# Optimization experiments

Hardware: AMD Instinct MI355X
Metric: run time of the kernel (lower is better)

Reference implementation:

```python
import jax, jax.numpy as jnp
import numpy as np
import math

EMBED_DIM = 2048
NUM_HEADS = 16
D_K = 128
BSZ = 2
SEQ = 2048


def make_freq_pos_enc(dim, max_seq_len):
    # inv_freq over dim/2 freqs, then interleave-repeat each freq twice: (f r), r=2
    inv_freq = 1.0 / (10000.0 ** (jnp.arange(0, dim, 2, dtype=jnp.float32) / dim))
    pos = jnp.arange(max_seq_len, dtype=jnp.float32)
    pe = jnp.einsum('p,f->pf', pos, inv_freq)                 # [S, dim/2]
    return jnp.repeat(pe, 2, axis=-1)                          # [S, dim], pattern (f r)


def rotate_half(u):
    # pairs are interleaved: (..., d r) with r=2
    u = u.reshape(*u.shape[:-1], -1, 2)
    u1, u2 = u[..., 0], u[..., 1]
    return jnp.stack((-u2, u1), axis=-1).reshape(*u.shape[:-2], -1)


def rotate(u, pos_enc):
    pe = pos_enc[: u.shape[-2]]                                # [S, d_k]
    return u * jnp.cos(pe) + rotate_half(u) * jnp.sin(pe)


def setup_inputs() -> dict:
    key = jax.random.key(0)
    ks = jax.random.split(key, 5)
    scale = 1.0 / math.sqrt(EMBED_DIM)
    return {
        'x': jax.random.normal(ks[0], (BSZ, SEQ, EMBED_DIM), dtype=jnp.float32),
        'wq': jax.random.normal(ks[1], (NUM_HEADS * D_K, EMBED_DIM), dtype=jnp.float32) * scale,
        'wk': jax.random.normal(ks[2], (NUM_HEADS * D_K, EMBED_DIM), dtype=jnp.float32) * scale,
        'wv': jax.random.normal(ks[3], (NUM_HEADS * D_K, EMBED_DIM), dtype=jnp.float32) * scale,
        'wo': jax.random.normal(ks[4], (EMBED_DIM, NUM_HEADS * D_K), dtype=jnp.float32) * scale,
        'freq_pos_enc': make_freq_pos_enc(D_K, SEQ),
        'mask': jnp.zeros((SEQ, SEQ), dtype=jnp.float32),  # dead arg in original forward
        'num_heads': NUM_HEADS,
        'd_k': D_K,
    }


def reference(x, wq, wk, wv, wo, freq_pos_enc, mask, num_heads, d_k):
    bsz, seq_len, _ = x.shape
    # projections (nn.Linear, no bias): x @ W^T
    def proj(w):
        p = jnp.einsum('bse,de->bsd', x, w)
        return p.reshape(bsz, seq_len, num_heads, d_k).transpose(0, 2, 1, 3)  # [B,H,S,d]
    q, k, v = proj(wq), proj(wk), proj(wv)
    q, k = rotate(q, freq_pos_enc), rotate(k, freq_pos_enc)
    # regenerated causal mask (0 on/below diagonal, -inf above)
    causal = jnp.where(
        jnp.arange(seq_len)[:, None] >= jnp.arange(seq_len)[None, :],
        0.0, -jnp.inf).astype(x.dtype)
    scores = jnp.einsum('bhsd,bhtd->bhst', q, k) / math.sqrt(d_k) + causal
    weights = jax.nn.softmax(scores, axis=-1)
    attn = jnp.einsum('bhst,bhtd->bhsd', weights, v)           # [B,H,S,d]
    attn = attn.transpose(0, 2, 1, 3).reshape(bsz, seq_len, -1)
    return jnp.einsum('bsd,ed->bse', attn, wo)


if __name__ == '__main__':
    out = reference(**setup_inputs())
    print(out.shape, out.dtype)
```

## Files before the change

kernel.cpp:

```cpp
#include <hip/hip_runtime.h>


typedef unsigned short u16;
typedef unsigned int   u32;
typedef __attribute__((ext_vector_type(4)))  float f32x4;
typedef __attribute__((ext_vector_type(16))) float f32x16;
typedef __attribute__((ext_vector_type(8)))  short short8;
typedef __attribute__((ext_vector_type(4)))  u16   u16x4;
typedef __attribute__((ext_vector_type(2)))  u16   u16x2;

#define NB   2
#define NH   16
#define SEQ  2048
#define DK   128
#define EMB  2048

__device__ __forceinline__ u16 f2bf(float f) {
    union { float f; unsigned int u; } v; v.f = f;
    unsigned int r = v.u + 0x7FFFu + ((v.u >> 16) & 1u);
    return (u16)(r >> 16);
}
__device__ __forceinline__ float bf2f(u16 h) {
    union { unsigned int u; float f; } v; v.u = ((unsigned int)h) << 16;
    return v.f;
}
__device__ __forceinline__ f32x4 mfma16(short8 a, short8 b, f32x4 c) {
    return __builtin_amdgcn_mfma_f32_16x16x32_bf16(a, b, c, 0, 0, 0);
}
__device__ __forceinline__ f32x16 mfma32(short8 a, short8 b, f32x16 c) {
    return __builtin_amdgcn_mfma_f32_32x32x16_bf16(a, b, c, 0, 0, 0);
}

#define GLDS(gsrc, ldst) __builtin_amdgcn_global_load_lds( \
    (const __attribute__((address_space(1))) void*)(gsrc), \
    (__attribute__((address_space(3))) void*)(ldst), 16, 0, 0)

__global__ __launch_bounds__(256) void cast_f32_bf16(const float* __restrict__ in,
                                                     u16* __restrict__ out, int n4) {
    int i = blockIdx.x * 256 + threadIdx.x;
    if (i >= n4) return;
    f32x4 v = ((const f32x4*)in)[i];
    u16x4 o;
    o[0] = f2bf(v[0]); o[1] = f2bf(v[1]); o[2] = f2bf(v[2]); o[3] = f2bf(v[3]);
    ((u16x4*)out)[i] = o;
}

__global__ __launch_bounds__(256) void rope_table(const float* __restrict__ freq,
                                                  float* __restrict__ ct,
                                                  float* __restrict__ st) {
    int i = blockIdx.x * 256 + threadIdx.x;
    int s = i >> 6, d2 = i & 63;
    float pe = freq[s * DK + d2 * 2];
    ct[i] = cosf(pe);
    st[i] = sinf(pe);
}

__global__ __launch_bounds__(256) void rope_apply(u16* __restrict__ Qb, u16* __restrict__ Kb,
                                                  const float* __restrict__ ct,
                                                  const float* __restrict__ st) {
    int i = blockIdx.x * 256 + threadIdx.x;
    int d2 = i & 63;
    int s  = (i >> 6) & (SEQ - 1);
    float c  = ct[(s << 6) + d2];
    float sn = st[(s << 6) + d2];
    size_t off = (size_t)i * 2;
    u16x2 q = *(const u16x2*)(Qb + off);
    float q0 = bf2f(q[0]), q1 = bf2f(q[1]);
    u16x2 qo; qo[0] = f2bf(q0 * c - q1 * sn); qo[1] = f2bf(q1 * c + q0 * sn);
    *(u16x2*)(Qb + off) = qo;
    u16x2 k = *(const u16x2*)(Kb + off);
    float k0 = bf2f(k[0]), k1 = bf2f(k[1]);
    u16x2 ko; ko[0] = f2bf(k0 * c - k1 * sn); ko[1] = f2bf(k1 * c + k0 * sn);
    *(u16x2*)(Kb + off) = ko;
}

template <int MODE>
__global__ __launch_bounds__(256) void gemm_ring(const u16* __restrict__ A,
                                                 const u16* __restrict__ B,
                                                 void* __restrict__ Cout,
                                                 int M, int N, int K) {
    __shared__ __align__(16) u16 As[3 * 4096];
    __shared__ __align__(16) u16 Bs[3 * 4096];
    const int tid  = threadIdx.x;
    const int lane = tid & 63;
    const int wid  = tid >> 6;
    const int wm   = wid >> 1, wn = wid & 1;
    const int nwgx = (int)gridDim.x;
    const int wgid = (int)blockIdx.y * nwgx + (int)blockIdx.x;
    const int cpx  = (nwgx * (int)gridDim.y) >> 3;
    const int swz  = (wgid & 7) * cpx + (wgid >> 3);
    const int m0   = (swz % nwgx) * 128, n0 = (swz / nwgx) * 128;
    const int lr   = lane & 15, lk = lane >> 4;

    const u16* Asrc = A + (size_t)(m0 + (tid >> 2)) * K + (tid & 3) * 8;
    const u16* Bsrc = B + (size_t)(n0 + (tid >> 2)) * K + (tid & 3) * 8;
    const int  dst0 = wid * 512;

    f32x4 acc[4][4] = {};
    const int NT = K >> 5;

#pragma unroll
    for (int i = 0; i < 2; ++i) {
        GLDS(Asrc + (size_t)i * 64 * K,      &As[i * 2048 + dst0]);
        GLDS(Bsrc + (size_t)i * 64 * K,      &Bs[i * 2048 + dst0]);
    }
#pragma unroll
    for (int i = 0; i < 2; ++i) {
        GLDS(Asrc + (size_t)i * 64 * K + 32, &As[4096 + i * 2048 + dst0]);
        GLDS(Bsrc + (size_t)i * 64 * K + 32, &Bs[4096 + i * 2048 + dst0]);
    }

    int buf = 0;
    for (int t = 0; t < NT; ++t) {
        if (t < NT - 1) asm volatile("s_waitcnt vmcnt(4)" ::: "memory");
        else            asm volatile("s_waitcnt vmcnt(0)" ::: "memory");
        __builtin_amdgcn_s_barrier();

        short8 af[4], bf[4];
#pragma unroll
        for (int i = 0; i < 4; ++i)
            af[i] = *(const short8*)&As[buf * 4096 + (wm * 64 + i * 16 + lr) * 32 + lk * 8];
#pragma unroll
        for (int j = 0; j < 4; ++j)
            bf[j] = *(const short8*)&Bs[buf * 4096 + (wn * 64 + j * 16 + lr) * 32 + lk * 8];

        if (t + 2 < NT) {
            int b2 = buf + 2; if (b2 >= 3) b2 -= 3;
            const u16* a2  = Asrc + (size_t)(t + 2) * 32;
            const u16* b2p = Bsrc + (size_t)(t + 2) * 32;
#pragma unroll
            for (int i = 0; i < 2; ++i) {
                GLDS(a2  + (size_t)i * 64 * K, &As[b2 * 4096 + i * 2048 + dst0]);
                GLDS(b2p + (size_t)i * 64 * K, &Bs[b2 * 4096 + i * 2048 + dst0]);
            }
        }

        __builtin_amdgcn_s_setprio(1);
#pragma unroll
        for (int i = 0; i < 4; ++i)
#pragma unroll
            for (int j = 0; j < 4; ++j)
                acc[i][j] = mfma16(af[i], bf[j], acc[i][j]);
        __builtin_amdgcn_s_setprio(0);

        buf = (buf == 2) ? 0 : buf + 1;
    }

#pragma unroll
    for (int i = 0; i < 4; ++i) {
#pragma unroll
        for (int j = 0; j < 4; ++j) {
#pragma unroll
            for (int r = 0; r < 4; ++r) {
                int m = m0 + wm * 64 + i * 16 + lk * 4 + r;
                int n = n0 + wn * 64 + j * 16 + lr;
                float v = acc[i][j][r];
                if (MODE == 0) {
                    int b = m >> 11, s = m & (SEQ - 1), h = n >> 7, d = n & (DK - 1);
                    ((u16*)Cout)[(((size_t)(b * NH + h) * SEQ + s) * DK) + d] = f2bf(v);
                } else if (MODE == 1) {
                    int h = m >> 7, d = m & (DK - 1), b = n >> 11, s = n & (SEQ - 1);
                    ((u16*)Cout)[(((size_t)(b * NH + h) * DK + d) * SEQ) + s] = f2bf(v);
                } else {
                    ((float*)Cout)[(size_t)m * N + n] = v;
                }
            }
        }
    }
}

__global__ __launch_bounds__(64, 2) void attn_lds(const u16* __restrict__ Q,
                                                  const u16* __restrict__ K,
                                                  const u16* __restrict__ VT,
                                                  u16* __restrict__ O) {
    const int gid  = blockIdx.x;
    const int bh   = (gid & 7) * 4 + ((gid >> 3) & 3);
    const int p    = gid >> 5;
    const int l    = threadIdx.x;
    const int q32  = l & 31;
    const int half = l >> 5;

    __shared__ __align__(16) u16 Ksh[2][4096];
    __shared__ __align__(16) u16 Vsh[2][4096];

    const u16* Kg  = K  + (size_t)bh * SEQ * DK;
    const u16* VTg = VT + (size_t)bh * DK * SEQ;
    const int b = bh >> 4, h = bh & 15;

    auto stage = [&](int t, int bufn) {
#pragma unroll
        for (int i = 0; i < 8; ++i) {
            int cid = i * 64 + l;
            int kr = cid >> 4, kc = cid & 15;
            GLDS(Kg + (size_t)(t * 32 + kr) * DK + ((kc ^ (kr & 7)) * 8),
                 &Ksh[bufn][i * 512]);
            int vr = cid >> 2, vc = cid & 3;
            GLDS(VTg + (size_t)vr * SEQ + t * 32 + ((vc ^ ((vr >> 1) & 3)) * 8),
                 &Vsh[bufn][i * 512]);
        }
    };

    auto process = [&](int qc) {
        const int q0 = qc * 32;
        const int nt = qc + 1;
        const u16* Qg = Q + ((size_t)bh * SEQ + q0) * DK;

        short8 qf[8];
#pragma unroll
        for (int kq = 0; kq < 8; ++kq)
            qf[kq] = *(const short8*)(Qg + q32 * DK + kq * 16 + half * 8);

        f32x16 oacc[4] = {};
        float m = -INFINITY, lsum = 0.f;

        stage(0, 0);
        for (int t = 0; t < nt; ++t) {
            const int buf = t & 1;
            if (t + 1 < nt) {
                stage(t + 1, (t + 1) & 1);
                asm volatile("s_waitcnt vmcnt(16)" ::: "memory");
            } else {
                asm volatile("s_waitcnt vmcnt(0)" ::: "memory");
            }
            __builtin_amdgcn_sched_barrier(0);

            const float rs = 0.08838834764831845f;
            short8 kf[8], vf[8];
#pragma unroll
            for (int kq = 0; kq < 8; ++kq) {
                int c = (kq * 2 + half) ^ (q32 & 7);
                kf[kq] = *(const short8*)&Ksh[buf][q32 * 128 + c * 8];
            }
#pragma unroll
            for (int i = 0; i < 8; ++i) {
                int dblk = i >> 1, ch = i & 1;
                int vrow = dblk * 32 + q32;
                int c = (ch * 2 + half) ^ ((q32 >> 1) & 3);
                vf[i] = *(const short8*)&Vsh[buf][vrow * 32 + c * 8];
            }
            const bool diag = (t == qc);

            f32x16 sacc = {};
            __builtin_amdgcn_s_setprio(1);
#pragma unroll
            for (int kq = 0; kq < 8; ++kq) sacc = mfma32(kf[kq], qf[kq], sacc);
            __builtin_amdgcn_s_setprio(0);
            float tmax = -INFINITY;
#pragma unroll
            for (int r = 0; r < 16; ++r) {
                int kk = (r & 3) + 8 * (r >> 2) + 4 * half;
                float s = sacc[r] * rs;
                if (diag && kk > q32) s = -INFINITY;
                sacc[r] = s;
                tmax = fmaxf(tmax, s);
            }
            tmax = fmaxf(tmax, __shfl_xor(tmax, 32));
            if (__any(tmax - m > 8.0f)) {
                float mn = fmaxf(m, tmax);
                float sc = __expf(m - mn);
                m = mn; lsum *= sc;
#pragma unroll
                for (int d = 0; d < 4; ++d)
#pragma unroll
                    for (int r = 0; r < 16; ++r) oacc[d][r] *= sc;
            }
            float tsum = 0.f;
#pragma unroll
            for (int r = 0; r < 16; ++r) { sacc[r] = __expf(sacc[r] - m); tsum += sacc[r]; }
            tsum += __shfl_xor(tsum, 32);
            lsum += tsum;
            u32 pk[8];
#pragma unroll
            for (int i = 0; i < 8; ++i)
                pk[i] = ((u32)f2bf(sacc[2 * i + 1]) << 16) | (u32)f2bf(sacc[2 * i]);
            u32 s0 = __shfl_xor((int)pk[0], 32), s1 = __shfl_xor((int)pk[1], 32);
            u32 s2 = __shfl_xor((int)pk[2], 32), s3 = __shfl_xor((int)pk[3], 32);
            u32 s4 = __shfl_xor((int)pk[4], 32), s5 = __shfl_xor((int)pk[5], 32);
            u32 s6 = __shfl_xor((int)pk[6], 32), s7 = __shfl_xor((int)pk[7], 32);
            union { u32 wd[4]; short8 s8; } P0, P1;
            P0.wd[0] = half ? s2    : pk[0];  P0.wd[1] = half ? s3    : pk[1];
            P0.wd[2] = half ? pk[2] : s0;     P0.wd[3] = half ? pk[3] : s1;
            P1.wd[0] = half ? s6    : pk[4];  P1.wd[1] = half ? s7    : pk[5];
            P1.wd[2] = half ? pk[6] : s4;     P1.wd[3] = half ? pk[7] : s5;
            __builtin_amdgcn_s_setprio(1);
#pragma unroll
            for (int d = 0; d < 4; ++d) {
                oacc[d] = mfma32(vf[2 * d],     P0.s8, oacc[d]);
                oacc[d] = mfma32(vf[2 * d + 1], P1.s8, oacc[d]);
            }
            __builtin_amdgcn_s_setprio(0);
        }

        float inv = 1.0f / lsum;
        u16* Og = O + ((size_t)b * SEQ + q0 + q32) * EMB + h * DK;
#pragma unroll
        for (int d = 0; d < 4; ++d)
#pragma unroll
            for (int rq = 0; rq < 4; ++rq) {
                u16x4 o4;
#pragma unroll
                for (int j = 0; j < 4; ++j) o4[j] = f2bf(oacc[d][rq * 4 + j] * inv);
                *(u16x4*)(Og + d * 32 + rq * 8 + half * 4) = o4;
            }
    };

    process(63 - p);
    process(p);
}

extern "C" void kernel_launch(void* const* d_in, const int* in_sizes, int n_in,
                              void* d_out, int out_size, void* d_ws, size_t ws_size,
                              hipStream_t stream) {
    const float* x    = (const float*)d_in[0];
    const float* wq   = (const float*)d_in[1];
    const float* wk   = (const float*)d_in[2];
    const float* wv   = (const float*)d_in[3];
    const float* wo   = (const float*)d_in[4];
    const float* freq = (const float*)d_in[5];

    char* ws = (char*)d_ws;
    u16*  xb  = (u16*)(ws);
    u16*  wqb = (u16*)(ws + 16777216);
    u16*  wkb = (u16*)(ws + 25165824);
    u16*  wvb = (u16*)(ws + 33554432);
    u16*  wob = (u16*)(ws + 41943040);
    u16*  Qb  = (u16*)(ws + 50331648);
    u16*  Kb  = (u16*)(ws + 67108864);
    u16*  VTb = (u16*)(ws + 83886080);
    float* ct = (float*)(ws + 100663296);
    float* st = (float*)(ws + 101187584);
    u16*  attn = xb;

    cast_f32_bf16<<<8192, 256, 0, stream>>>(x,  xb,  2097152);
    cast_f32_bf16<<<4096, 256, 0, stream>>>(wq, wqb, 1048576);
    cast_f32_bf16<<<4096, 256, 0, stream>>>(wk, wkb, 1048576);
    cast_f32_bf16<<<4096, 256, 0, stream>>>(wv, wvb, 1048576);
    cast_f32_bf16<<<4096, 256, 0, stream>>>(wo, wob, 1048576);
    rope_table<<<512, 256, 0, stream>>>(freq, ct, st);

    gemm_ring<0><<<dim3(32, 16), 256, 0, stream>>>(xb,  wqb, Qb,  4096, 2048, 2048);
    gemm_ring<0><<<dim3(32, 16), 256, 0, stream>>>(xb,  wkb, Kb,  4096, 2048, 2048);
    gemm_ring<1><<<dim3(16, 32), 256, 0, stream>>>(wvb, xb,  VTb, 2048, 4096, 2048);

    rope_apply<<<16384, 256, 0, stream>>>(Qb, Kb, ct, st);

    attn_lds<<<1024, 64, 0, stream>>>(Qb, Kb, VTb, attn);

    gemm_ring<3><<<dim3(32, 16), 256, 0, stream>>>(attn, wob, d_out, 4096, 2048, 2048);
}
```

Baseline: 305.0 us.

## Process paired query chunks in one pass sharing K/V tile loads

Instead of running the long and short query chunks sequentially, each with its own K/V streaming loop, the attention kernel now holds both chunks' Q fragments and accumulators and walks the K/V tiles once. The short chunk's update is applied only while its causal range is active. This cuts LDS staging and global K/V traffic for the short chunk and gives more MFMA work per staged tile. The cost is roughly double the register pressure (two sets of oacc and qf) at launch bounds 64,2, which could spill or lower occupancy. The max and sum reductions were also rewritten as trees.

```diff
diff --git a/kernel.cpp b/kernel.cpp
--- a/kernel.cpp
+++ b/kernel.cpp
@@ -176,6 +176,7 @@
     const int gid  = blockIdx.x;
     const int bh   = (gid & 7) * 4 + ((gid >> 3) & 3);
     const int p    = gid >> 5;
+    const int qcL  = 63 - p, qcS = p;
     const int l    = threadIdx.x;
     const int q32  = l & 31;
     const int half = l >> 5;
@@ -200,112 +201,138 @@
         }
     };
 
-    auto process = [&](int qc) {
-        const int q0 = qc * 32;
-        const int nt = qc + 1;
-        const u16* Qg = Q + ((size_t)bh * SEQ + q0) * DK;
-
-        short8 qf[8];
-#pragma unroll
-        for (int kq = 0; kq < 8; ++kq)
-            qf[kq] = *(const short8*)(Qg + q32 * DK + kq * 16 + half * 8);
-
-        f32x16 oacc[4] = {};
-        float m = -INFINITY, lsum = 0.f;
-
-        stage(0, 0);
-        for (int t = 0; t < nt; ++t) {
-            const int buf = t & 1;
-            if (t + 1 < nt) {
-                stage(t + 1, (t + 1) & 1);
-                asm volatile("s_waitcnt vmcnt(16)" ::: "memory");
-            } else {
-                asm volatile("s_waitcnt vmcnt(0)" ::: "memory");
-            }
-            __builtin_amdgcn_sched_barrier(0);
-
-            const float rs = 0.08838834764831845f;
-            short8 kf[8], vf[8];
-#pragma unroll
-            for (int kq = 0; kq < 8; ++kq) {
-                int c = (kq * 2 + half) ^ (q32 & 7);
-                kf[kq] = *(const short8*)&Ksh[buf][q32 * 128 + c * 8];
-            }
-#pragma unroll
-            for (int i = 0; i < 8; ++i) {
-                int dblk = i >> 1, ch = i & 1;
-                int vrow = dblk * 32 + q32;
-                int c = (ch * 2 + half) ^ ((q32 >> 1) & 3);
-                vf[i] = *(const short8*)&Vsh[buf][vrow * 32 + c * 8];
-            }
-            const bool diag = (t == qc);
-
-            f32x16 sacc = {};
-            __builtin_amdgcn_s_setprio(1);
-#pragma unroll
-            for (int kq = 0; kq < 8; ++kq) sacc = mfma32(kf[kq], qf[kq], sacc);
-            __builtin_amdgcn_s_setprio(0);
-            float tmax = -INFINITY;
-#pragma unroll
-            for (int r = 0; r < 16; ++r) {
-                int kk = (r & 3) + 8 * (r >> 2) + 4 * half;
-                float s = sacc[r] * rs;
-                if (diag && kk > q32) s = -INFINITY;
-                sacc[r] = s;
-                tmax = fmaxf(tmax, s);
-            }
-            tmax = fmaxf(tmax, __shfl_xor(tmax, 32));
-            if (__any(tmax - m > 8.0f)) {
-                float mn = fmaxf(m, tmax);
-                float sc = __expf(m - mn);
-                m = mn; lsum *= sc;
-#pragma unroll
-                for (int d = 0; d < 4; ++d)
-#pragma unroll
-                    for (int r = 0; r < 16; ++r) oacc[d][r] *= sc;
-            }
-            float tsum = 0.f;
-#pragma unroll
-            for (int r = 0; r < 16; ++r) { sacc[r] = __expf(sacc[r] - m); tsum += sacc[r]; }
-            tsum += __shfl_xor(tsum, 32);
-            lsum += tsum;
-            u32 pk[8];
-#pragma unroll
-            for (int i = 0; i < 8; ++i)
-                pk[i] = ((u32)f2bf(sacc[2 * i + 1]) << 16) | (u32)f2bf(sacc[2 * i]);
-            u32 s0 = __shfl_xor((int)pk[0], 32), s1 = __shfl_xor((int)pk[1], 32);
-            u32 s2 = __shfl_xor((int)pk[2], 32), s3 = __shfl_xor((int)pk[3], 32);
-            u32 s4 = __shfl_xor((int)pk[4], 32), s5 = __shfl_xor((int)pk[5], 32);
-            u32 s6 = __shfl_xor((int)pk[6], 32), s7 = __shfl_xor((int)pk[7], 32);
-            union { u32 wd[4]; short8 s8; } P0, P1;
-            P0.wd[0] = half ? s2    : pk[0];  P0.wd[1] = half ? s3    : pk[1];
-            P0.wd[2] = half ? pk[2] : s0;     P0.wd[3] = half ? pk[3] : s1;
-            P1.wd[0] = half ? s6    : pk[4];  P1.wd[1] = half ? s7    : pk[5];
-            P1.wd[2] = half ? pk[6] : s4;     P1.wd[3] = half ? pk[7] : s5;
-            __builtin_amdgcn_s_setprio(1);
-#pragma unroll
-            for (int d = 0; d < 4; ++d) {
-                oacc[d] = mfma32(vf[2 * d],     P0.s8, oacc[d]);
-                oacc[d] = mfma32(vf[2 * d + 1], P1.s8, oacc[d]);
-            }
-            __builtin_amdgcn_s_setprio(0);
-        }
-
-        float inv = 1.0f / lsum;
-        u16* Og = O + ((size_t)b * SEQ + q0 + q32) * EMB + h * DK;
+    short8 qfL[8], qfS[8];
+    {
+        const u16* QgL = Q + ((size_t)bh * SEQ + qcL * 32) * DK;
+        const u16* QgS = Q + ((size_t)bh * SEQ + qcS * 32) * DK;
+#pragma unroll
+        for (int kq = 0; kq < 8; ++kq) {
+            qfL[kq] = *(const short8*)(QgL + q32 * DK + kq * 16 + half * 8);
+            qfS[kq] = *(const short8*)(QgS + q32 * DK + kq * 16 + half * 8);
+        }
+    }
+
+    f32x16 oL[4] = {}, oS[4] = {};
+    float mL = -INFINITY, mS = -INFINITY, lL = 0.f, lS = 0.f;
+
+    auto chunkStep = [&](short8 (&qf)[8], f32x16 (&oacc)[4], float& m, float& lsum,
+                         short8 (&kf)[8], short8 (&vf)[8], bool diag) {
+        const float rs = 0.08838834764831845f;
+        f32x16 sacc = {};
+        __builtin_amdgcn_s_setprio(1);
+#pragma unroll
+        for (int kq = 0; kq < 8; ++kq) sacc = mfma32(kf[kq], qf[kq], sacc);
+        __builtin_amdgcn_s_setprio(0);
+#pragma unroll
+        for (int r = 0; r < 16; ++r) {
+            int kk = (r & 3) + 8 * (r >> 2) + 4 * half;
+            float s = sacc[r] * rs;
+            if (diag && kk > q32) s = -INFINITY;
+            sacc[r] = s;
+        }
+        float mx[8];
+#pragma unroll
+        for (int r = 0; r < 8; ++r) mx[r] = fmaxf(sacc[r], sacc[r + 8]);
+#pragma unroll
+        for (int r = 0; r < 4; ++r) mx[r] = fmaxf(mx[r], mx[r + 4]);
+        float tmax = fmaxf(fmaxf(mx[0], mx[1]), fmaxf(mx[2], mx[3]));
+        tmax = fmaxf(tmax, __shfl_xor(tmax, 32));
+        if (__any(tmax - m > 8.0f)) {
+            float mn = fmaxf(m, tmax);
+            float sc = __expf(m - mn);
+            m = mn; lsum *= sc;
+#pragma unroll
+            for (int d = 0; d < 4; ++d)
+#pragma unroll
+                for (int r = 0; r < 16; ++r) oacc[d][r] *= sc;
+        }
+#pragma unroll
+        for (int r = 0; r < 16; ++r) sacc[r] = __expf(sacc[r] - m);
+        float sm[8];
+#pragma unroll
+        for (int r = 0; r < 8; ++r) sm[r] = sacc[r] + sacc[r + 8];
+#pragma unroll
+        for (int r = 0; r < 4; ++r) sm[r] = sm[r] + sm[r + 4];
+        float tsum = (sm[0] + sm[1]) + (sm[2] + sm[3]);
+        tsum += __shfl_xor(tsum, 32);
+        lsum += tsum;
+        u32 pk[8];
+#pragma unroll
+        for (int i = 0; i < 8; ++i)
+            pk[i] = ((u32)f2bf(sacc[2 * i + 1]) << 16) | (u32)f2bf(sacc[2 * i]);
+        u32 s0 = __shfl_xor((int)pk[0], 32), s1 = __shfl_xor((int)pk[1], 32);
+        u32 s2 = __shfl_xor((int)pk[2], 32), s3 = __shfl_xor((int)pk[3], 32);
+        u32 s4 = __shfl_xor((int)pk[4], 32), s5 = __shfl_xor((int)pk[5], 32);
+        u32 s6 = __shfl_xor((int)pk[6], 32), s7 = __shfl_xor((int)pk[7], 32);
+        union { u32 wd[4]; short8 s8; } P0, P1;
+        P0.wd[0] = half ? s2    : pk[0];  P0.wd[1] = half ? s3    : pk[1];
+        P0.wd[2] = half ? pk[2] : s0;     P0.wd[3] = half ? pk[3] : s1;
+        P1.wd[0] = half ? s6    : pk[4];  P1.wd[1] = half ? s7    : pk[5];
+        P1.wd[2] = half ? pk[6] : s4;     P1.wd[3] = half ? pk[7] : s5;
+        __builtin_amdgcn_s_setprio(1);
+#pragma unroll
+        for (int d = 0; d < 4; ++d) {
+            oacc[d] = mfma32(vf[2 * d],     P0.s8, oacc[d]);
+            oacc[d] = mfma32(vf[2 * d + 1], P1.s8, oacc[d]);
+        }
+        __builtin_amdgcn_s_setprio(0);
+    };
+
+    stage(0, 0);
+    for (int t = 0; t <= qcL; ++t) {
+        const int buf = t & 1;
+        if (t < qcL) {
+            stage(t + 1, (t + 1) & 1);
+            asm volatile("s_waitcnt vmcnt(16)" ::: "memory");
+        } else {
+            asm volatile("s_waitcnt vmcnt(0)" ::: "memory");
+        }
+        __builtin_amdgcn_sched_barrier(0);
+
+        short8 kf[8], vf[8];
+#pragma unroll
+        for (int kq = 0; kq < 8; ++kq) {
+            int c = (kq * 2 + half) ^ (q32 & 7);
+            kf[kq] = *(const short8*)&Ksh[buf][q32 * 128 + c * 8];
+        }
+#pragma unroll
+        for (int i = 0; i < 8; ++i) {
+            int dblk = i >> 1, ch = i & 1;
+            int vrow = dblk * 32 + q32;
+            int c = (ch * 2 + half) ^ ((q32 >> 1) & 3);
+            vf[i] = *(const short8*)&Vsh[buf][vrow * 32 + c * 8];
+        }
+
+        chunkStep(qfL, oL, mL, lL, kf, vf, t == qcL);
+        if (t <= qcS) chunkStep(qfS, oS, mS, lS, kf, vf, t == qcS);
+    }
+
+    {
+        float inv = 1.0f / lL;
+        u16* Og = O + ((size_t)b * SEQ + qcL * 32 + q32) * EMB + h * DK;
 #pragma unroll
         for (int d = 0; d < 4; ++d)
 #pragma unroll
             for (int rq = 0; rq < 4; ++rq) {
                 u16x4 o4;
 #pragma unroll
-                for (int j = 0; j < 4; ++j) o4[j] = f2bf(oacc[d][rq * 4 + j] * inv);
+                for (int j = 0; j < 4; ++j) o4[j] = f2bf(oL[d][rq * 4 + j] * inv);
                 *(u16x4*)(Og + d * 32 + rq * 8 + half * 4) = o4;
             }
-    };
-
-    process(63 - p);
-    process(p);
+    }
+    {
+        float inv = 1.0f / lS;
+        u16* Og = O + ((size_t)b * SEQ + qcS * 32 + q32) * EMB + h * DK;
+#pragma unroll
+        for (int d = 0; d < 4; ++d)
+#pragma unroll
+            for (int rq = 0; rq < 4; ++rq) {
+                u16x4 o4;
+#pragma unroll
+                for (int j = 0; j < 4; ++j) o4[j] = f2bf(oS[d][rq * 4 + j] * inv);
+                *(u16x4*)(Og + d * 32 + rq * 8 + half * 4) = o4;
+            }
+    }
 }
 
 extern "C" void kernel_launch(void* const* d_in, const int* in_sizes, int n_in,
```

Measured after the change: 392.1 us. 28.6% more time.

## Split attention block into two waves sharing K/V tiles across paired query chunks

Applied to the files above, without the earlier changes.

The attention kernel now runs two wavefronts per block, one handling the long query chunk and one the short query chunk, instead of one wave processing both chunks in sequence. Both waves share the same staged K/V tiles in LDS, so the short chunk's tiles are loaded once rather than twice, and the staging work is split across the two waves. The pipeline is restructured to prefetch two tiles ahead, with block barriers around each buffer reuse. The max and sum reductions become tree reductions. The short-chunk wave idles for the remaining tiles while still hitting the barriers, and the added barriers introduce synchronisation cost.

```diff
diff --git a/kernel.cpp b/kernel.cpp
--- a/kernel.cpp
+++ b/kernel.cpp
@@ -169,16 +169,22 @@
     }
 }
 
-__global__ __launch_bounds__(64, 2) void attn_lds(const u16* __restrict__ Q,
-                                                  const u16* __restrict__ K,
-                                                  const u16* __restrict__ VT,
-                                                  u16* __restrict__ O) {
+__global__ __launch_bounds__(128, 2) void attn_lds2(const u16* __restrict__ Q,
+                                                    const u16* __restrict__ K,
+                                                    const u16* __restrict__ VT,
+                                                    u16* __restrict__ O) {
     const int gid  = blockIdx.x;
     const int bh   = (gid & 7) * 4 + ((gid >> 3) & 3);
     const int p    = gid >> 5;
-    const int l    = threadIdx.x;
+    const int tid  = threadIdx.x;
+    const int w    = tid >> 6;
+    const int l    = tid & 63;
     const int q32  = l & 31;
     const int half = l >> 5;
+    const int qcL  = 63 - p;
+    const int qc   = w ? p : qcL;
+    const int nt   = qcL + 1;
+    const int q0   = qc * 32;
 
     __shared__ __align__(16) u16 Ksh[2][4096];
     __shared__ __align__(16) u16 Vsh[2][4096];
@@ -189,41 +195,38 @@
 
     auto stage = [&](int t, int bufn) {
 #pragma unroll
-        for (int i = 0; i < 8; ++i) {
-            int cid = i * 64 + l;
+        for (int i = 0; i < 4; ++i) {
+            int cid = i * 128 + w * 64 + l;
             int kr = cid >> 4, kc = cid & 15;
             GLDS(Kg + (size_t)(t * 32 + kr) * DK + ((kc ^ (kr & 7)) * 8),
-                 &Ksh[bufn][i * 512]);
+                 &Ksh[bufn][(i * 128 + w * 64) * 8]);
             int vr = cid >> 2, vc = cid & 3;
             GLDS(VTg + (size_t)vr * SEQ + t * 32 + ((vc ^ ((vr >> 1) & 3)) * 8),
-                 &Vsh[bufn][i * 512]);
+                 &Vsh[bufn][(i * 128 + w * 64) * 8]);
         }
     };
 
-    auto process = [&](int qc) {
-        const int q0 = qc * 32;
-        const int nt = qc + 1;
+    short8 qf[8];
+    {
         const u16* Qg = Q + ((size_t)bh * SEQ + q0) * DK;
-
-        short8 qf[8];
 #pragma unroll
         for (int kq = 0; kq < 8; ++kq)
             qf[kq] = *(const short8*)(Qg + q32 * DK + kq * 16 + half * 8);
-
-        f32x16 oacc[4] = {};
-        float m = -INFINITY, lsum = 0.f;
-
-        stage(0, 0);
-        for (int t = 0; t < nt; ++t) {
-            const int buf = t & 1;
-            if (t + 1 < nt) {
-                stage(t + 1, (t + 1) & 1);
-                asm volatile("s_waitcnt vmcnt(16)" ::: "memory");
-            } else {
-                asm volatile("s_waitcnt vmcnt(0)" ::: "memory");
-            }
-            __builtin_amdgcn_sched_barrier(0);
-
+    }
+
+    f32x16 oacc[4] = {};
+    float m = -INFINITY, lsum = 0.f;
+
+    stage(0, 0);
+    stage(1, 1);
+    for (int t = 0; t < nt; ++t) {
+        const int buf = t & 1;
+        if (t + 1 < nt) asm volatile("s_waitcnt vmcnt(8)" ::: "memory");
+        else            asm volatile("s_waitcnt vmcnt(0)" ::: "memory");
+        __builtin_amdgcn_s_barrier();
+        __builtin_amdgcn_sched_barrier(0);
+
+        if (t <= qc) {
             const float rs = 0.08838834764831845f;
             short8 kf[8], vf[8];
 #pragma unroll
@@ -245,15 +248,19 @@
 #pragma unroll
             for (int kq = 0; kq < 8; ++kq) sacc = mfma32(kf[kq], qf[kq], sacc);
             __builtin_amdgcn_s_setprio(0);
-            float tmax = -INFINITY;
 #pragma unroll
             for (int r = 0; r < 16; ++r) {
                 int kk = (r & 3) + 8 * (r >> 2) + 4 * half;
                 float s = sacc[r] * rs;
                 if (diag && kk > q32) s = -INFINITY;
                 sacc[r] = s;
-                tmax = fmaxf(tmax, s);
-            }
+            }
+            float mx[8];
+#pragma unroll
+            for (int r = 0; r < 8; ++r) mx[r] = fmaxf(sacc[r], sacc[r + 8]);
+#pragma unroll
+            for (int r = 0; r < 4; ++r) mx[r] = fmaxf(mx[r], mx[r + 4]);
+            float tmax = fmaxf(fmaxf(mx[0], mx[1]), fmaxf(mx[2], mx[3]));
             tmax = fmaxf(tmax, __shfl_xor(tmax, 32));
             if (__any(tmax - m > 8.0f)) {
                 float mn = fmaxf(m, tmax);
@@ -264,9 +271,14 @@
 #pragma unroll
                     for (int r = 0; r < 16; ++r) oacc[d][r] *= sc;
             }
-            float tsum = 0.f;
-#pragma unroll
-            for (int r = 0; r < 16; ++r) { sacc[r] = __expf(sacc[r] - m); tsum += sacc[r]; }
+#pragma unroll
+            for (int r = 0; r < 16; ++r) sacc[r] = __expf(sacc[r] - m);
+            float sm[8];
+#pragma unroll
+            for (int r = 0; r < 8; ++r) sm[r] = sacc[r] + sacc[r + 8];
+#pragma unroll
+            for (int r = 0; r < 4; ++r) sm[r] = sm[r] + sm[r + 4];
+            float tsum = (sm[0] + sm[1]) + (sm[2] + sm[3]);
             tsum += __shfl_xor(tsum, 32);
             lsum += tsum;
             u32 pk[8];
@@ -291,21 +303,21 @@
             __builtin_amdgcn_s_setprio(0);
         }
 
-        float inv = 1.0f / lsum;
-        u16* Og = O + ((size_t)b * SEQ + q0 + q32) * EMB + h * DK;
-#pragma unroll
-        for (int d = 0; d < 4; ++d)
-#pragma unroll
-            for (int rq = 0; rq < 4; ++rq) {
-                u16x4 o4;
-#pragma unroll
-                for (int j = 0; j < 4; ++j) o4[j] = f2bf(oacc[d][rq * 4 + j] * inv);
-                *(u16x4*)(Og + d * 32 + rq * 8 + half * 4) = o4;
-            }
-    };
-
-    process(63 - p);
-    process(p);
+        __builtin_amdgcn_s_barrier();
+        if (t + 2 < nt) stage(t + 2, buf);
+    }
+
+    float inv = 1.0f / lsum;
+    u16* Og = O + ((size_t)b * SEQ + q0 + q32) * EMB + h * DK;
+#pragma unroll
+    for (int d = 0; d < 4; ++d)
+#pragma unroll
+        for (int rq = 0; rq < 4; ++rq) {
+            u16x4 o4;
+#pragma unroll
+            for (int j = 0; j < 4; ++j) o4[j] = f2bf(oacc[d][rq * 4 + j] * inv);
+            *(u16x4*)(Og + d * 32 + rq * 8 + half * 4) = o4;
+        }
 }
 
 extern "C" void kernel_launch(void* const* d_in, const int* in_sizes, int n_in,
@@ -344,7 +356,7 @@
 
     rope_apply<<<16384, 256, 0, stream>>>(Qb, Kb, ct, st);
 
-    attn_lds<<<1024, 64, 0, stream>>>(Qb, Kb, VTb, attn);
+    attn_lds2<<<1024, 128, 0, stream>>>(Qb, Kb, VTb, attn);
 
     gemm_ring<3><<<dim3(32, 16), 256, 0, stream>>>(attn, wob, d_out, 4096, 2048, 2048);
 }
```

Result: faster. 294.5 us (-3.4%).
